# Performance work log

Measured on AMD Instinct MI355X. Metric: run time of the kernel, lower is better.

The kernel has to match this reference:

```python
import jax, jax.numpy as jnp
import numpy as np

HIDDEN = 3072
NUM_HEADS = 24
HEAD_DIM = HIDDEN // NUM_HEADS  # 128
MLP_HIDDEN = 4 * HIDDEN         # 12288
SEQ = 2048


def setup_inputs() -> dict:
    key = jax.random.key(0)
    ks = jax.random.split(key, 12)
    s = 0.02
    return {
        "x": jax.random.normal(ks[0], (1, SEQ, HIDDEN), jnp.float32),
        "vec": jax.random.normal(ks[1], (1, HIDDEN), jnp.float32),
        "pe": jax.random.normal(ks[2], (1, 1, SEQ, HEAD_DIM // 2, 2, 2), jnp.float32),
        "mod_w": jax.random.normal(ks[3], (HIDDEN, 3 * HIDDEN), jnp.float32) * s,
        "mod_b": jnp.zeros((3 * HIDDEN,), jnp.float32),
        "lin1_w": jax.random.normal(ks[4], (HIDDEN, 3 * HIDDEN + MLP_HIDDEN), jnp.float32) * s,
        "lin1_b": jnp.zeros((3 * HIDDEN + MLP_HIDDEN,), jnp.float32),
        "lin2_w": jax.random.normal(ks[5], (HIDDEN + MLP_HIDDEN, HIDDEN), jnp.float32) * s,
        "lin2_b": jnp.zeros((HIDDEN,), jnp.float32),
        "q_scale": jnp.ones((HEAD_DIM,), jnp.float32),
        "k_scale": jnp.ones((HEAD_DIM,), jnp.float32),
    }


def _forward(x, vec, pe, mod_w, mod_b, lin1_w, lin1_b, lin2_w, lin2_b, q_scale, k_scale):
    B, L, H = x.shape
    NH, HD = NUM_HEADS, HEAD_DIM

    # Modulation: lin(silu(vec)) -> shift, scale, gate  (flux Modulation, double=False)
    mod = jnp.dot(jax.nn.silu(vec), mod_w) + mod_b          # (B, 3H)
    shift, scale, gate = jnp.split(mod, 3, axis=-1)
    shift, scale, gate = shift[:, None, :], scale[:, None, :], gate[:, None, :]

    # LayerNorm (no affine, eps=1e-6) + scale/shift modulation
    mu = jnp.mean(x, axis=-1, keepdims=True)
    var = jnp.mean((x - mu) ** 2, axis=-1, keepdims=True)
    xn = (x - mu) * jax.lax.rsqrt(var + 1e-6)
    x_mod = (1.0 + scale) * xn + shift

    # Fused QKV + MLP projection
    h = jnp.dot(x_mod, lin1_w) + lin1_b                     # (B, L, 3H + MLP)
    qkv, mlp = h[..., : 3 * H], h[..., 3 * H :]
    qkv = qkv.reshape(B, L, 3, NH, HD).transpose(2, 0, 3, 1, 4)  # (3, B, NH, L, HD)
    q, k, v = qkv[0], qkv[1], qkv[2]

    # QKNorm: RMSNorm over head_dim with learned scale (eps=1e-6)
    def rms(t, s):
        return t * jax.lax.rsqrt(jnp.mean(t * t, axis=-1, keepdims=True) + 1e-6) * s

    q = rms(q, q_scale)
    k = rms(k, k_scale)

    # Rotary embedding: pe is (B, 1, L, HD/2, 2, 2) of rotation matrix rows
    def rope(t):
        tr = t.reshape(B, NH, L, HD // 2, 1, 2)
        out = pe[..., 0] * tr[..., 0] + pe[..., 1] * tr[..., 1]  # (B, NH, L, HD/2, 2)
        return out.reshape(B, NH, L, HD)

    q, k = rope(q), rope(k)

    # Scaled dot-product attention (default 1/sqrt(HD) scale)
    scores = jnp.einsum("bhqd,bhkd->bhqk", q, k) / jnp.sqrt(jnp.float32(HD))
    attn = jnp.einsum("bhqk,bhkd->bhqd", jax.nn.softmax(scores, axis=-1), v)
    attn = attn.transpose(0, 2, 1, 3).reshape(B, L, H)

    # GELU(tanh) MLP branch, concat, output projection, gated residual
    mlp_act = jax.nn.gelu(mlp, approximate=True)
    out = jnp.dot(jnp.concatenate([attn, mlp_act], axis=-1), lin2_w) + lin2_b
    return x + gate * out


def reference(x, vec, pe, mod_w, mod_b, lin1_w, lin1_b, lin2_w, lin2_b, q_scale, k_scale):
    return _forward(x, vec, pe, mod_w, mod_b, lin1_w, lin1_b, lin2_w, lin2_b, q_scale, k_scale)
```

## Files before the change

### kernel.cpp

```cpp
#include <hip/hip_runtime.h>
#include <hip/hip_bf16.h>
#include <stdint.h>

#define SEQ   2048
#define HID   3072
#define NHEADS 24
#define HDIM  128
#define MLPD  12288
#define NCOL1 21504
#define NCOL2 15360
#define MOD3  9216
#define QKVW  9216
#define KSPLIT 8

typedef __attribute__((ext_vector_type(4))) float f32x4;
typedef __attribute__((ext_vector_type(8))) short bf16x8;
typedef __attribute__((ext_vector_type(4))) unsigned short u16x4;
typedef __attribute__((ext_vector_type(2))) unsigned short u16x2;

__device__ __forceinline__ unsigned short f2bf(float f){
  unsigned u = __float_as_uint(f);
  u = (u + 0x7fffu + ((u >> 16) & 1u)) >> 16;
  return (unsigned short)u;
}
__device__ __forceinline__ float bf2f(unsigned short u){
  return __uint_as_float(((unsigned)u) << 16);
}

__device__ __forceinline__ void gload_lds16(const void* g, void* l){
  __builtin_amdgcn_global_load_lds(
      (const __attribute__((address_space(1))) unsigned int*)g,
      (__attribute__((address_space(3))) unsigned int*)l, 16, 0, 0);
}

__device__ __forceinline__ float gelu_tanh(float x){
  float u = 0.7978845608028654f * (x + 0.044715f * x * x * x);
  float t = 1.f - 2.f / (__expf(2.f * u) + 1.f);
  return 0.5f * x * (1.f + t);
}

__global__ void silu_kernel(const float* __restrict__ vec, float* __restrict__ sv){
  int i = blockIdx.x * 256 + threadIdx.x;
  if (i < HID){ float v = vec[i]; sv[i] = v / (1.f + __expf(-v)); }
}

__global__ void mod_gemv(const float* __restrict__ sv, const float* __restrict__ W,
                         const float* __restrict__ b, float* __restrict__ mod){
  int n  = blockIdx.x * 32 + (threadIdx.x & 31);
  int ks = threadIdx.x >> 5;
  float acc = 0.f;
  int k0 = ks * 384;
  #pragma unroll 4
  for (int k = k0; k < k0 + 384; ++k)
    acc += sv[k] * W[(size_t)k * MOD3 + n];
  __shared__ float red[8][32];
  red[ks][threadIdx.x & 31] = acc;
  __syncthreads();
  if (ks == 0){
    float a = 0.f;
    #pragma unroll
    for (int i = 0; i < 8; ++i) a += red[i][threadIdx.x & 31];
    mod[n] = a + b[n];
  }
}

__global__ __launch_bounds__(256)
void ln_mod_kernel(const float* __restrict__ x, const float* __restrict__ mod,
                   unsigned short* __restrict__ xmod){
  int l = blockIdx.x, t = threadIdx.x;
  const float* row = x + (size_t)l * HID;
  f32x4 v[3];
  float s = 0.f, s2 = 0.f;
  #pragma unroll
  for (int i = 0; i < 3; ++i){
    v[i] = *(const f32x4*)(row + (t + i * 256) * 4);
    #pragma unroll
    for (int j = 0; j < 4; ++j){ s += v[i][j]; s2 += v[i][j] * v[i][j]; }
  }
  #pragma unroll
  for (int m = 1; m < 64; m <<= 1){ s += __shfl_xor(s, m, 64); s2 += __shfl_xor(s2, m, 64); }
  __shared__ float red[8];
  int wv = t >> 6, ln = t & 63;
  if (ln == 0){ red[wv] = s; red[4 + wv] = s2; }
  __syncthreads();
  s  = red[0] + red[1] + red[2] + red[3];
  s2 = red[4] + red[5] + red[6] + red[7];
  float mu  = s * (1.f / HID);
  float var = s2 * (1.f / HID) - mu * mu;
  float rs  = rsqrtf(var + 1e-6f);
  #pragma unroll
  for (int i = 0; i < 3; ++i){
    int c = (t + i * 256) * 4;
    f32x4 sh = *(const f32x4*)(mod + c);
    f32x4 sc = *(const f32x4*)(mod + HID + c);
    u16x4 o;
    #pragma unroll
    for (int j = 0; j < 4; ++j){
      float xn = (v[i][j] - mu) * rs;
      o[j] = f2bf((1.f + sc[j]) * xn + sh[j]);
    }
    *(u16x4*)(xmod + (size_t)l * HID + c) = o;
  }
}

__global__ __launch_bounds__(256)
void transpose_f2b(const float* __restrict__ in, unsigned short* __restrict__ out,
                   int R, int C){
  __shared__ float tile[64][65];
  int rt = blockIdx.y * 64, ct = blockIdx.x * 64;
  int t = threadIdx.x;
  int r0 = t >> 4, c0 = (t & 15) * 4;
  #pragma unroll
  for (int ph = 0; ph < 4; ++ph){
    int r = r0 + ph * 16;
    f32x4 v = *(const f32x4*)(in + (size_t)(rt + r) * C + ct + c0);
    tile[r][c0 + 0] = v[0]; tile[r][c0 + 1] = v[1];
    tile[r][c0 + 2] = v[2]; tile[r][c0 + 3] = v[3];
  }
  __syncthreads();
  #pragma unroll
  for (int ph = 0; ph < 4; ++ph){
    int r = r0 + ph * 16;
    u16x4 o;
    #pragma unroll
    for (int i = 0; i < 4; ++i) o[i] = f2bf(tile[c0 + i][r]);
    *(u16x4*)(out + (size_t)(ct + r) * R + rt + c0) = o;
  }
}

__global__ __launch_bounds__(256)
void transpose_b2b_head(const unsigned short* __restrict__ in,
                        unsigned short* __restrict__ out, int R, int C){
  __shared__ unsigned short tile[64][68];
  int h = blockIdx.z;
  const unsigned short* inh = in + (size_t)h * R * C;
  unsigned short* outh = out + (size_t)h * R * C;
  int rt = blockIdx.y * 64, ct = blockIdx.x * 64;
  int t = threadIdx.x;
  int r0 = t >> 4, c0 = (t & 15) * 4;
  #pragma unroll
  for (int ph = 0; ph < 4; ++ph){
    int r = r0 + ph * 16;
    u16x4 v = *(const u16x4*)(inh + (size_t)(rt + r) * C + ct + c0);
    tile[r][c0 + 0] = v[0]; tile[r][c0 + 1] = v[1];
    tile[r][c0 + 2] = v[2]; tile[r][c0 + 3] = v[3];
  }
  __syncthreads();
  #pragma unroll
  for (int ph = 0; ph < 4; ++ph){
    int r = r0 + ph * 16;
    u16x4 o;
    #pragma unroll
    for (int i = 0; i < 4; ++i) o[i] = tile[c0 + i][r];
    *(u16x4*)(outh + (size_t)(ct + r) * R + rt + c0) = o;
  }
}

__global__ void qkv_prep(const unsigned short* __restrict__ hq, const float* __restrict__ pe,
                         const float* __restrict__ qscale, const float* __restrict__ kscale,
                         unsigned short* __restrict__ qb, unsigned short* __restrict__ kb,
                         unsigned short* __restrict__ vb){
  int l = blockIdx.x, hh = blockIdx.y, lane = threadIdx.x;
  const unsigned short* row = hq + (size_t)l * QKVW;
  int d = lane * 2;
  u16x2 qv = *(const u16x2*)(row + hh * HDIM + d);
  u16x2 kv = *(const u16x2*)(row + HID + hh * HDIM + d);
  u16x2 vv = *(const u16x2*)(row + 2 * HID + hh * HDIM + d);
  float qx = bf2f(qv[0]), qy = bf2f(qv[1]);
  float kx = bf2f(kv[0]), ky = bf2f(kv[1]);
  float sq = qx * qx + qy * qy;
  float sk = kx * kx + ky * ky;
  #pragma unroll
  for (int m = 1; m < 64; m <<= 1){ sq += __shfl_xor(sq, m, 64); sk += __shfl_xor(sk, m, 64); }
  float rq = rsqrtf(sq * (1.f / HDIM) + 1e-6f);
  float rk = rsqrtf(sk * (1.f / HDIM) + 1e-6f);
  float2 qs2 = *(const float2*)(qscale + d);
  float2 ks2 = *(const float2*)(kscale + d);
  float q0 = qx * rq * qs2.x, q1 = qy * rq * qs2.y;
  float k0 = kx * rk * ks2.x, k1 = ky * rk * ks2.y;
  f32x4 p4 = *(const f32x4*)(pe + (size_t)l * 256 + lane * 4);
  const float sscl = 0.08838834764831845f;
  float qo0 = (p4[0] * q0 + p4[1] * q1) * sscl;
  float qo1 = (p4[2] * q0 + p4[3] * q1) * sscl;
  float ko0 =  p4[0] * k0 + p4[1] * k1;
  float ko1 =  p4[2] * k0 + p4[3] * k1;
  size_t base = ((size_t)hh * SEQ + l) * HDIM + d;
  u16x2 o;
  o[0] = f2bf(qo0); o[1] = f2bf(qo1); *(u16x2*)(qb + base) = o;
  o[0] = f2bf(ko0); o[1] = f2bf(ko1); *(u16x2*)(kb + base) = o;
  o[0] = vv[0];     o[1] = vv[1];     *(u16x2*)(vb + base) = o;
}

template<int EPI>
__global__ __launch_bounds__(512)
void gemm256(const unsigned short* __restrict__ A, const unsigned short* __restrict__ BT,
             const float* __restrict__ bias, unsigned short* __restrict__ out0,
             unsigned short* __restrict__ out1,
             int M, int N, int ldA, int ldB, int kchunk){
  __shared__ unsigned short Ls[65536];
  int nxy = gridDim.x * gridDim.y;
  int nwg = nxy * gridDim.z;
  int fid = (blockIdx.z * gridDim.y + blockIdx.y) * gridDim.x + blockIdx.x;
  int nid = (fid & 7) * (nwg >> 3) + (fid >> 3);
  int ksz = nid / nxy, rem = nid % nxy;
  int bm  = rem % gridDim.y, bn = rem / gridDim.y;
  int k0 = ksz * kchunk;
  int nk = kchunk >> 6;
  int tid = threadIdx.x, wave = tid >> 6, lane = tid & 63, lg = lane >> 4, lr = lane & 15;
  int wr = wave >> 2, wc = wave & 3;

  int G0 = tid, G1 = tid + 512;
  int r0 = G0 >> 2, r1 = G1 >> 2;
  int c0 = ((G0 & 3) ^ ((r0 >> 1) & 3)) * 8;
  int c1 = ((G1 & 3) ^ ((r1 >> 1) & 3)) * 8;
  const unsigned short* A0 = A  + (size_t)(bm * 256 + r0) * ldA + k0 + c0;
  const unsigned short* A1 = A  + (size_t)(bm * 256 + r1) * ldA + k0 + c1;
  const unsigned short* B0 = BT + (size_t)(bn * 256 + r0) * ldB + k0 + c0;
  const unsigned short* B1 = BT + (size_t)(bn * 256 + r1) * ldB + k0 + c1;
  unsigned short* LA = Ls;
  unsigned short* LB = Ls + 32768;
  int d0 = (wave * 64) * 8, d1 = (512 + wave * 64) * 8;

  auto stageA = [&](int t, int kh){
    unsigned short* h = LA + (((t & 1) * 2 + kh) << 13);
    int kc = t * 64 + kh * 32;
    gload_lds16(A0 + kc, h + d0);
    gload_lds16(A1 + kc, h + d1);
  };
  auto stageB = [&](int t, int kh){
    unsigned short* h = LB + (((t & 1) * 2 + kh) << 13);
    int kc = t * 64 + kh * 32;
    gload_lds16(B0 + kc, h + d0);
    gload_lds16(B1 + kc, h + d1);
  };

  int offA[8], offB[4];
  #pragma unroll
  for (int m = 0; m < 8; ++m){
    int row = wr * 128 + m * 16 + lr;
    offA[m] = row * 32 + ((lg ^ ((row >> 1) & 3)) * 8);
  }
  #pragma unroll
  for (int n = 0; n < 4; ++n){
    int row = wc * 64 + n * 16 + lr;
    offB[n] = row * 32 + ((lg ^ ((row >> 1) & 3)) * 8);
  }

  const f32x4 fz = 0.0f;
  f32x4 acc[8][4];
  #pragma unroll
  for (int i = 0; i < 8; ++i)
    #pragma unroll
    for (int j = 0; j < 4; ++j) acc[i][j] = fz;

  stageA(0, 0); stageB(0, 0); stageA(0, 1); stageB(0, 1); stageA(1, 0); stageB(1, 0);
  asm volatile("s_waitcnt vmcnt(8)" ::: "memory");
  __builtin_amdgcn_s_barrier();
  __builtin_amdgcn_sched_barrier(0);

  for (int t = 0; t < nk; ++t){
    const unsigned short* Ah = LA + (((t & 1) * 2) << 13);
    const unsigned short* Bh = LB + (((t & 1) * 2) << 13);
    bf16x8 a_[4], b_[4];
    if (t + 1 < nk) stageA(t + 1, 1);
    #pragma unroll
    for (int m = 0; m < 4; ++m) a_[m] = *(const bf16x8*)&Ah[offA[m]];
    #pragma unroll
    for (int n = 0; n < 4; ++n) b_[n] = *(const bf16x8*)&Bh[offB[n]];
    __builtin_amdgcn_sched_barrier(0);
    __builtin_amdgcn_s_barrier();
    asm volatile("s_waitcnt lgkmcnt(0)" ::: "memory");
    __builtin_amdgcn_sched_barrier(0);
    __builtin_amdgcn_s_setprio(1);
    #pragma unroll
    for (int m = 0; m < 4; ++m)
      #pragma unroll
      for (int n = 0; n < 4; ++n)
        acc[m][n] = __builtin_amdgcn_mfma_f32_16x16x32_bf16(a_[m], b_[n], acc[m][n], 0, 0, 0);
    __builtin_amdgcn_s_setprio(0);
    __builtin_amdgcn_sched_barrier(0);
    __builtin_amdgcn_s_barrier();
    if (t + 1 < nk) stageB(t + 1, 1);
    #pragma unroll
    for (int m = 0; m < 4; ++m) a_[m] = *(const bf16x8*)&Ah[offA[m + 4]];
    __builtin_amdgcn_sched_barrier(0);
    if (t == nk - 1) asm volatile("s_waitcnt vmcnt(0)" ::: "memory");
    else             asm volatile("s_waitcnt vmcnt(8)" ::: "memory");
    __builtin_amdgcn_s_barrier();
    asm volatile("s_waitcnt lgkmcnt(0)" ::: "memory");
    __builtin_amdgcn_sched_barrier(0);
    __builtin_amdgcn_s_setprio(1);
    #pragma unroll
    for (int m = 0; m < 4; ++m)
      #pragma unroll
      for (int n = 0; n < 4; ++n)
        acc[m + 4][n] = __builtin_amdgcn_mfma_f32_16x16x32_bf16(a_[m], b_[n], acc[m + 4][n], 0, 0, 0);
    __builtin_amdgcn_s_setprio(0);
    __builtin_amdgcn_sched_barrier(0);
    __builtin_amdgcn_s_barrier();
    if (t + 2 < nk) stageA(t + 2, 0);
    #pragma unroll
    for (int m = 0; m < 4; ++m) a_[m] = *(const bf16x8*)&Ah[8192 + offA[m]];
    #pragma unroll
    for (int n = 0; n < 4; ++n) b_[n] = *(const bf16x8*)&Bh[8192 + offB[n]];
    __builtin_amdgcn_sched_barrier(0);
    __builtin_amdgcn_s_barrier();
    asm volatile("s_waitcnt lgkmcnt(0)" ::: "memory");
    __builtin_amdgcn_sched_barrier(0);
    __builtin_amdgcn_s_setprio(1);
    #pragma unroll
    for (int m = 0; m < 4; ++m)
      #pragma unroll
      for (int n = 0; n < 4; ++n)
        acc[m][n] = __builtin_amdgcn_mfma_f32_16x16x32_bf16(a_[m], b_[n], acc[m][n], 0, 0, 0);
    __builtin_amdgcn_s_setprio(0);
    __builtin_amdgcn_sched_barrier(0);
    __builtin_amdgcn_s_barrier();
    if (t + 2 < nk) stageB(t + 2, 0);
    #pragma unroll
    for (int m = 0; m < 4; ++m) a_[m] = *(const bf16x8*)&Ah[8192 + offA[m + 4]];
    __builtin_amdgcn_sched_barrier(0);
    if (t <= nk - 3)      asm volatile("s_waitcnt vmcnt(8)" ::: "memory");
    else if (t == nk - 2) asm volatile("s_waitcnt vmcnt(4)" ::: "memory");
    __builtin_amdgcn_s_barrier();
    asm volatile("s_waitcnt lgkmcnt(0)" ::: "memory");
    __builtin_amdgcn_sched_barrier(0);
    __builtin_amdgcn_s_setprio(1);
    #pragma unroll
    for (int m = 0; m < 4; ++m)
      #pragma unroll
      for (int n = 0; n < 4; ++n)
        acc[m + 4][n] = __builtin_amdgcn_mfma_f32_16x16x32_bf16(a_[m], b_[n], acc[m + 4][n], 0, 0, 0);
    __builtin_amdgcn_s_setprio(0);
    __builtin_amdgcn_sched_barrier(0);
    __builtin_amdgcn_s_barrier();
  }

  if constexpr (EPI == 0){
    if (bn < MOD3 / 256){
      #pragma unroll
      for (int m = 0; m < 8; ++m)
        #pragma unroll
        for (int n = 0; n < 4; ++n){
          int col = bn * 256 + wc * 64 + n * 16 + lr;
          float bv = bias[col];
          #pragma unroll
          for (int jj = 0; jj < 4; ++jj){
            int row = bm * 256 + wr * 128 + m * 16 + lg * 4 + jj;
            out0[(size_t)row * QKVW + col] = f2bf(acc[m][n][jj] + bv);
          }
        }
    } else {
      #pragma unroll
      for (int m = 0; m < 8; ++m)
        #pragma unroll
        for (int n = 0; n < 4; ++n){
          int col = bn * 256 + wc * 64 + n * 16 + lr;
          float bv = bias[col];
          #pragma unroll
          for (int jj = 0; jj < 4; ++jj){
            int row = bm * 256 + wr * 128 + m * 16 + lg * 4 + jj;
            out1[(size_t)row * NCOL2 + (col - 2 * HID)] = f2bf(gelu_tanh(acc[m][n][jj] + bv));
          }
        }
    }
  } else {
    unsigned short* P = out0 + (size_t)ksz * M * N;
    #pragma unroll
    for (int m = 0; m < 8; ++m)
      #pragma unroll
      for (int n = 0; n < 4; ++n){
        int col = bn * 256 + wc * 64 + n * 16 + lr;
        #pragma unroll
        for (int jj = 0; jj < 4; ++jj){
          int row = bm * 256 + wr * 128 + m * 16 + lg * 4 + jj;
          P[(size_t)row * N + col] = f2bf(acc[m][n][jj]);
        }
      }
  }
}

__global__ __launch_bounds__(256)
void reduce_lin2(const unsigned short* __restrict__ part, const float* __restrict__ x,
                 const float* __restrict__ gate, const float* __restrict__ bias,
                 float* __restrict__ out){
  int i4 = blockIdx.x * 256 + threadIdx.x;
  int c4 = i4 % (HID / 4);
  f32x4 s = 0.0f;
  #pragma unroll
  for (int ks = 0; ks < KSPLIT; ++ks){
    u16x4 p = *(const u16x4*)(part + (size_t)ks * SEQ * HID + (size_t)i4 * 4);
    #pragma unroll
    for (int j = 0; j < 4; ++j) s[j] += bf2f(p[j]);
  }
  f32x4 xv = *(const f32x4*)(x + (size_t)i4 * 4);
  f32x4 gv = *(const f32x4*)(gate + c4 * 4);
  f32x4 bv = *(const f32x4*)(bias + c4 * 4);
  f32x4 o;
  #pragma unroll
  for (int j = 0; j < 4; ++j) o[j] = xv[j] + gv[j] * (s[j] + bv[j]);
  *(f32x4*)(out + (size_t)i4 * 4) = o;
}

__global__ __launch_bounds__(256)
void attn_kernel(const unsigned short* __restrict__ qb, const unsigned short* __restrict__ kb,
                 const unsigned short* __restrict__ vt, unsigned short* __restrict__ a2){
  __shared__ unsigned short Ksm[64 * 128];
  __shared__ unsigned short Vsm[128 * 64];
  __shared__ unsigned short Psm[4][16 * 64];
  int fid = blockIdx.y * gridDim.x + blockIdx.x;
  int nid = (fid & 7) * 96 + (fid >> 3);
  int hh = nid / (SEQ / 64), qt = nid % (SEQ / 64);
  int tid = threadIdx.x, wave = tid >> 6, lane = tid & 63, lg = lane >> 4, lr = lane & 15;
  const unsigned short* Kh = kb + (size_t)hh * SEQ * HDIM;
  const unsigned short* Vh = vt + (size_t)hh * HDIM * SEQ;
  const unsigned short* Qh = qb + (size_t)hh * SEQ * HDIM;
  int q0 = qt * 64 + wave * 16;

  bf16x8 aq[4];
  #pragma unroll
  for (int kk = 0; kk < 4; ++kk)
    aq[kk] = *(const bf16x8*)(Qh + (size_t)(q0 + lr) * HDIM + kk * 32 + lg * 8);

  const f32x4 fzero = 0.0f;
  f32x4 acc_o[8];
  #pragma unroll
  for (int n = 0; n < 8; ++n) acc_o[n] = fzero;
  float mrun[4] = {-1e30f, -1e30f, -1e30f, -1e30f};
  float lrun[4] = {0.f, 0.f, 0.f, 0.f};

  for (int t = 0; t < SEQ / 64; ++t){
    __syncthreads();
    const unsigned short* Kt = Kh + (size_t)t * 64 * HDIM;
    const unsigned short* Vt = Vh + t * 64;
    #pragma unroll
    for (int r = 0; r < 4; ++r){
      int G  = r * 256 + tid;
      int Gs = G ^ ((G >> 4) & 7);
      gload_lds16(Kt + Gs * 8, (void*)&Ksm[(r * 256 + wave * 64) * 8]);
      int Gv = G ^ ((G >> 3) & 7);
      gload_lds16(Vt + (size_t)(Gv >> 3) * SEQ + (Gv & 7) * 8,
                  (void*)&Vsm[(r * 256 + wave * 64) * 8]);
    }
    __syncthreads();

    f32x4 sacc[4];
    #pragma unroll
    for (int j = 0; j < 4; ++j) sacc[j] = fzero;
    #pragma unroll
    for (int j = 0; j < 4; ++j){
      int kv = j * 16 + lr;
      #pragma unroll
      for (int kk = 0; kk < 4; ++kk){
        int bo = kv * 256 + (kk * 32 + lg * 8) * 2;
        bo ^= (kv & 7) << 4;
        bf16x8 bk = *(const bf16x8*)((const char*)Ksm + bo);
        sacc[j] = __builtin_amdgcn_mfma_f32_16x16x32_bf16(aq[kk], bk, sacc[j], 0, 0, 0);
      }
    }
    float scl[4], psum[4];
    #pragma unroll
    for (int jj = 0; jj < 4; ++jj){
      float m_ = fmaxf(fmaxf(sacc[0][jj], sacc[1][jj]), fmaxf(sacc[2][jj], sacc[3][jj]));
      #pragma unroll
      for (int mk = 1; mk < 16; mk <<= 1) m_ = fmaxf(m_, __shfl_xor(m_, mk, 64));
      float mn = fmaxf(mrun[jj], m_);
      scl[jj] = __expf(mrun[jj] - mn);
      mrun[jj] = mn;
      psum[jj] = 0.f;
    }
    #pragma unroll
    for (int j = 0; j < 4; ++j)
      #pragma unroll
      for (int jj = 0; jj < 4; ++jj){
        float p = __expf(sacc[j][jj] - mrun[jj]);
        sacc[j][jj] = p;
        psum[jj] += p;
      }
    #pragma unroll
    for (int jj = 0; jj < 4; ++jj){
      float ps = psum[jj];
      #pragma unroll
      for (int mk = 1; mk < 16; mk <<= 1) ps += __shfl_xor(ps, mk, 64);
      lrun[jj] = lrun[jj] * scl[jj] + ps;
    }
    #pragma unroll
    for (int n = 0; n < 8; ++n)
      #pragma unroll
      for (int jj = 0; jj < 4; ++jj) acc_o[n][jj] *= scl[jj];
    unsigned short* Pw = Psm[wave];
    #pragma unroll
    for (int j = 0; j < 4; ++j)
      #pragma unroll
      for (int jj = 0; jj < 4; ++jj){
        int prow = lg * 4 + jj, pcol = j * 16 + lr;
        int bo = prow * 128 + pcol * 2;
        bo ^= (prow & 7) << 4;
        *(unsigned short*)((char*)Pw + bo) = f2bf(sacc[j][jj]);
      }
    __syncthreads();
    #pragma unroll
    for (int k2 = 0; k2 < 2; ++k2){
      int bo = lr * 128 + (k2 * 32 + lg * 8) * 2;
      bo ^= (lr & 7) << 4;
      bf16x8 pf = *(const bf16x8*)((const char*)Pw + bo);
      #pragma unroll
      for (int n = 0; n < 8; ++n){
        int dd = n * 16 + lr;
        int vb_ = dd * 128 + (k2 * 32 + lg * 8) * 2;
        vb_ ^= (dd & 7) << 4;
        bf16x8 vf = *(const bf16x8*)((const char*)Vsm + vb_);
        acc_o[n] = __builtin_amdgcn_mfma_f32_16x16x32_bf16(pf, vf, acc_o[n], 0, 0, 0);
      }
    }
  }
  #pragma unroll
  for (int jj = 0; jj < 4; ++jj) lrun[jj] = 1.f / lrun[jj];
  #pragma unroll
  for (int n = 0; n < 8; ++n)
    #pragma unroll
    for (int jj = 0; jj < 4; ++jj){
      int row = q0 + lg * 4 + jj;
      int col = hh * HDIM + n * 16 + lr;
      a2[(size_t)row * NCOL2 + col] = f2bf(acc_o[n][jj] * lrun[jj]);
    }
}

extern "C" void kernel_launch(void* const* d_in, const int* in_sizes, int n_in,
                              void* d_out, int out_size, void* d_ws, size_t ws_size,
                              hipStream_t stream){
  const float* x       = (const float*)d_in[0];
  const float* vec     = (const float*)d_in[1];
  const float* pe      = (const float*)d_in[2];
  const float* mod_w   = (const float*)d_in[3];
  const float* mod_b   = (const float*)d_in[4];
  const float* lin1_w  = (const float*)d_in[5];
  const float* lin1_b  = (const float*)d_in[6];
  const float* lin2_w  = (const float*)d_in[7];
  const float* lin2_b  = (const float*)d_in[8];
  const float* q_scale = (const float*)d_in[9];
  const float* k_scale = (const float*)d_in[10];
  float* out = (float*)d_out;

  char* ws = (char*)d_ws;
  size_t off = 0;
  auto alloc = [&](size_t bytes){ void* p = ws + off; off += (bytes + 255) & ~(size_t)255; return p; };
  float* sv            = (float*)alloc((size_t)HID * 4);
  float* mod           = (float*)alloc((size_t)MOD3 * 4);
  unsigned short* xmod = (unsigned short*)alloc((size_t)SEQ * HID * 2);
  unsigned short* wt2  = (unsigned short*)alloc((size_t)HID * NCOL2 * 2);
  unsigned short* a2   = (unsigned short*)alloc((size_t)SEQ * NCOL2 * 2);
  unsigned short* qb   = (unsigned short*)alloc((size_t)NHEADS * SEQ * HDIM * 2);
  unsigned short* kb   = (unsigned short*)alloc((size_t)NHEADS * SEQ * HDIM * 2);
  unsigned short* vb   = (unsigned short*)alloc((size_t)NHEADS * SEQ * HDIM * 2);
  unsigned short* vt   = (unsigned short*)alloc((size_t)NHEADS * SEQ * HDIM * 2);
  unsigned short* wt1  = (unsigned short*)alloc((size_t)NCOL1 * HID * 2);
  unsigned short* hq   = (unsigned short*)alloc((size_t)SEQ * QKVW * 2);
  unsigned short* part = qb;

  silu_kernel<<<12, 256, 0, stream>>>(vec, sv);
  mod_gemv<<<MOD3 / 32, 256, 0, stream>>>(sv, mod_w, mod_b, mod);
  transpose_f2b<<<dim3(NCOL1 / 64, HID / 64), 256, 0, stream>>>(lin1_w, wt1, HID, NCOL1);
  transpose_f2b<<<dim3(HID / 64, NCOL2 / 64), 256, 0, stream>>>(lin2_w, wt2, NCOL2, HID);
  ln_mod_kernel<<<SEQ, 256, 0, stream>>>(x, mod, xmod);
  gemm256<0><<<dim3(NCOL1 / 256, SEQ / 256, 1), 512, 0, stream>>>(
      xmod, wt1, lin1_b, hq, a2, SEQ, NCOL1, HID, HID, HID);
  qkv_prep<<<dim3(SEQ, NHEADS), 64, 0, stream>>>(hq, pe, q_scale, k_scale, qb, kb, vb);
  transpose_b2b_head<<<dim3(HDIM / 64, SEQ / 64, NHEADS), 256, 0, stream>>>(vb, vt, SEQ, HDIM);
  attn_kernel<<<dim3(SEQ / 64, NHEADS), 256, 0, stream>>>(qb, kb, vt, a2);
  gemm256<2><<<dim3(HID / 256, SEQ / 256, KSPLIT), 512, 0, stream>>>(
      a2, wt2, nullptr, part, nullptr, SEQ, HID, NCOL2, NCOL2, NCOL2 / KSPLIT);
  reduce_lin2<<<SEQ * HID / 4 / 256, 256, 0, stream>>>(part, x, mod + 2 * HID, lin2_b, out);
}
```

Before: 847.1 us.

## Use 256x192 tiles for lin2 GEMM with split-K reduced to four

The GEMM kernel now takes the number of N-fragments per wave as a template parameter, so the lin2 projection uses 256x192 tiles (16 column tiles) with split-K of 4 in place of 256x256 tiles with split-K of 8. The B tile staging masks off the extra threads and adjusts the vmcnt waits to match. The aim is to halve the partial-sum traffic written by the GEMM and read by the reduction while keeping a similar workgroup count (512 rather than 768). In exchange each workgroup does fewer MFMAs per A-tile load, which lowers arithmetic intensity.

```diff
diff --git a/kernel.cpp b/kernel.cpp
--- a/kernel.cpp
+++ b/kernel.cpp
@@ -11,12 +11,14 @@
 #define NCOL2 15360
 #define MOD3  9216
 #define QKVW  9216
-#define KSPLIT 8
+#define KS2   4
 
 typedef __attribute__((ext_vector_type(4))) float f32x4;
 typedef __attribute__((ext_vector_type(8))) short bf16x8;
 typedef __attribute__((ext_vector_type(4))) unsigned short u16x4;
 typedef __attribute__((ext_vector_type(2))) unsigned short u16x2;
+
+#define VMC(n) asm volatile("s_waitcnt vmcnt(" #n ")" ::: "memory")
 
 __device__ __forceinline__ unsigned short f2bf(float f){
   unsigned u = __float_as_uint(f);
@@ -191,13 +193,17 @@
   o[0] = vv[0];     o[1] = vv[1];     *(u16x2*)(vb + base) = o;
 }
 
-template<int EPI>
+template<int NFRAG, int EPI>
 __global__ __launch_bounds__(512)
 void gemm256(const unsigned short* __restrict__ A, const unsigned short* __restrict__ BT,
              const float* __restrict__ bias, unsigned short* __restrict__ out0,
              unsigned short* __restrict__ out1,
              int M, int N, int ldA, int ldB, int kchunk){
-  __shared__ unsigned short Ls[65536];
+  constexpr int BN  = NFRAG * 64;
+  constexpr int BGT = BN * 2;
+  constexpr int HB  = BN * 32;
+  __shared__ unsigned short As[4 * 8192];
+  __shared__ unsigned short Bs[4 * HB];
   int nxy = gridDim.x * gridDim.y;
   int nwg = nxy * gridDim.z;
   int fid = (blockIdx.z * gridDim.y + blockIdx.y) * gridDim.x + blockIdx.x;
@@ -209,64 +215,67 @@
   int tid = threadIdx.x, wave = tid >> 6, lane = tid & 63, lg = lane >> 4, lr = lane & 15;
   int wr = wave >> 2, wc = wave & 3;
 
-  int G0 = tid, G1 = tid + 512;
-  int r0 = G0 >> 2, r1 = G1 >> 2;
-  int c0 = ((G0 & 3) ^ ((r0 >> 1) & 3)) * 8;
-  int c1 = ((G1 & 3) ^ ((r1 >> 1) & 3)) * 8;
-  const unsigned short* A0 = A  + (size_t)(bm * 256 + r0) * ldA + k0 + c0;
-  const unsigned short* A1 = A  + (size_t)(bm * 256 + r1) * ldA + k0 + c1;
-  const unsigned short* B0 = BT + (size_t)(bn * 256 + r0) * ldB + k0 + c0;
-  const unsigned short* B1 = BT + (size_t)(bn * 256 + r1) * ldB + k0 + c1;
-  unsigned short* LA = Ls;
-  unsigned short* LB = Ls + 32768;
+  int rA0 = tid >> 2, rA1 = (tid + 512) >> 2;
+  int cA0 = ((tid & 3) ^ ((rA0 >> 1) & 3)) * 8;
+  int cA1 = ((tid & 3) ^ ((rA1 >> 1) & 3)) * 8;
+  const unsigned short* A0 = A + (size_t)(bm * 256 + rA0) * ldA + k0 + cA0;
+  const unsigned short* A1 = A + (size_t)(bm * 256 + rA1) * ldA + k0 + cA1;
+  int rB0 = tid >> 2, rB1 = (tid + BGT) >> 2;
+  int cB1 = ((tid & 3) ^ ((rB1 >> 1) & 3)) * 8;
+  const unsigned short* B0 = BT + (size_t)(bn * BN + rB0) * ldB + k0 + cA0;
+  const unsigned short* B1 = BT + (size_t)(bn * BN + rB1) * ldB + k0 + cB1;
   int d0 = (wave * 64) * 8, d1 = (512 + wave * 64) * 8;
+  int dB1 = (BGT + wave * 64) * 8;
+  bool bact = (BGT == 512) || (tid < BGT);
 
   auto stageA = [&](int t, int kh){
-    unsigned short* h = LA + (((t & 1) * 2 + kh) << 13);
+    unsigned short* h = As + (((t & 1) * 2 + kh) << 13);
     int kc = t * 64 + kh * 32;
     gload_lds16(A0 + kc, h + d0);
     gload_lds16(A1 + kc, h + d1);
   };
   auto stageB = [&](int t, int kh){
-    unsigned short* h = LB + (((t & 1) * 2 + kh) << 13);
-    int kc = t * 64 + kh * 32;
-    gload_lds16(B0 + kc, h + d0);
-    gload_lds16(B1 + kc, h + d1);
+    if (bact){
+      unsigned short* h = Bs + ((t & 1) * 2 + kh) * HB;
+      int kc = t * 64 + kh * 32;
+      gload_lds16(B0 + kc, h + d0);
+      gload_lds16(B1 + kc, h + dB1);
+    }
   };
 
-  int offA[8], offB[4];
+  int offA[8], offB[NFRAG];
   #pragma unroll
   for (int m = 0; m < 8; ++m){
     int row = wr * 128 + m * 16 + lr;
     offA[m] = row * 32 + ((lg ^ ((row >> 1) & 3)) * 8);
   }
   #pragma unroll
-  for (int n = 0; n < 4; ++n){
-    int row = wc * 64 + n * 16 + lr;
+  for (int n = 0; n < NFRAG; ++n){
+    int row = wc * (NFRAG * 16) + n * 16 + lr;
     offB[n] = row * 32 + ((lg ^ ((row >> 1) & 3)) * 8);
   }
 
   const f32x4 fz = 0.0f;
-  f32x4 acc[8][4];
+  f32x4 acc[8][NFRAG];
   #pragma unroll
   for (int i = 0; i < 8; ++i)
     #pragma unroll
-    for (int j = 0; j < 4; ++j) acc[i][j] = fz;
+    for (int j = 0; j < NFRAG; ++j) acc[i][j] = fz;
 
   stageA(0, 0); stageB(0, 0); stageA(0, 1); stageB(0, 1); stageA(1, 0); stageB(1, 0);
-  asm volatile("s_waitcnt vmcnt(8)" ::: "memory");
+  if (bact) VMC(8); else VMC(4);
   __builtin_amdgcn_s_barrier();
   __builtin_amdgcn_sched_barrier(0);
 
   for (int t = 0; t < nk; ++t){
-    const unsigned short* Ah = LA + (((t & 1) * 2) << 13);
-    const unsigned short* Bh = LB + (((t & 1) * 2) << 13);
-    bf16x8 a_[4], b_[4];
+    const unsigned short* Ah = As + (((t & 1) * 2) << 13);
+    const unsigned short* Bh = Bs + ((t & 1) * 2) * HB;
+    bf16x8 a_[4], b_[NFRAG];
     if (t + 1 < nk) stageA(t + 1, 1);
     #pragma unroll
     for (int m = 0; m < 4; ++m) a_[m] = *(const bf16x8*)&Ah[offA[m]];
     #pragma unroll
-    for (int n = 0; n < 4; ++n) b_[n] = *(const bf16x8*)&Bh[offB[n]];
+    for (int n = 0; n < NFRAG; ++n) b_[n] = *(const bf16x8*)&Bh[offB[n]];
     __builtin_amdgcn_sched_barrier(0);
     __builtin_amdgcn_s_barrier();
     asm volatile("s_waitcnt lgkmcnt(0)" ::: "memory");
@@ -275,7 +284,7 @@
     #pragma unroll
     for (int m = 0; m < 4; ++m)
       #pragma unroll
-      for (int n = 0; n < 4; ++n)
+      for (int n = 0; n < NFRAG; ++n)
         acc[m][n] = __builtin_amdgcn_mfma_f32_16x16x32_bf16(a_[m], b_[n], acc[m][n], 0, 0, 0);
     __builtin_amdgcn_s_setprio(0);
     __builtin_amdgcn_sched_barrier(0);
@@ -284,8 +293,8 @@
     #pragma unroll
     for (int m = 0; m < 4; ++m) a_[m] = *(const bf16x8*)&Ah[offA[m + 4]];
     __builtin_amdgcn_sched_barrier(0);
-    if (t == nk - 1) asm volatile("s_waitcnt vmcnt(0)" ::: "memory");
-    else             asm volatile("s_waitcnt vmcnt(8)" ::: "memory");
+    if (t == nk - 1){ VMC(0); }
+    else            { if (bact) VMC(8); else VMC(4); }
     __builtin_amdgcn_s_barrier();
     asm volatile("s_waitcnt lgkmcnt(0)" ::: "memory");
     __builtin_amdgcn_sched_barrier(0);
@@ -293,7 +302,7 @@
     #pragma unroll
     for (int m = 0; m < 4; ++m)
       #pragma unroll
-      for (int n = 0; n < 4; ++n)
+      for (int n = 0; n < NFRAG; ++n)
         acc[m + 4][n] = __builtin_amdgcn_mfma_f32_16x16x32_bf16(a_[m], b_[n], acc[m + 4][n], 0, 0, 0);
     __builtin_amdgcn_s_setprio(0);
     __builtin_amdgcn_sched_barrier(0);
@@ -302,7 +311,7 @@
     #pragma unroll
     for (int m = 0; m < 4; ++m) a_[m] = *(const bf16x8*)&Ah[8192 + offA[m]];
     #pragma unroll
-    for (int n = 0; n < 4; ++n) b_[n] = *(const bf16x8*)&Bh[8192 + offB[n]];
+    for (int n = 0; n < NFRAG; ++n) b_[n] = *(const bf16x8*)&Bh[HB + offB[n]];
     __builtin_amdgcn_sched_barrier(0);
     __builtin_amdgcn_s_barrier();
     asm volatile("s_waitcnt lgkmcnt(0)" ::: "memory");
@@ -311,7 +320,7 @@
     #pragma unroll
     for (int m = 0; m < 4; ++m)
       #pragma unroll
-      for (int n = 0; n < 4; ++n)
+      for (int n = 0; n < NFRAG; ++n)
         acc[m][n] = __builtin_amdgcn_mfma_f32_16x16x32_bf16(a_[m], b_[n], acc[m][n], 0, 0, 0);
     __builtin_amdgcn_s_setprio(0);
     __builtin_amdgcn_sched_barrier(0);
@@ -320,8 +329,8 @@
     #pragma unroll
     for (int m = 0; m < 4; ++m) a_[m] = *(const bf16x8*)&Ah[8192 + offA[m + 4]];
     __builtin_amdgcn_sched_barrier(0);
-    if (t <= nk - 3)      asm volatile("s_waitcnt vmcnt(8)" ::: "memory");
-    else if (t == nk - 2) asm volatile("s_waitcnt vmcnt(4)" ::: "memory");
+    if (t <= nk - 3)      { if (bact) VMC(8); else VMC(4); }
+    else if (t == nk - 2) { if (bact) VMC(4); else VMC(2); }
     __builtin_amdgcn_s_barrier();
     asm volatile("s_waitcnt lgkmcnt(0)" ::: "memory");
     __builtin_amdgcn_sched_barrier(0);
@@ -329,7 +338,7 @@
     #pragma unroll
     for (int m = 0; m < 4; ++m)
       #pragma unroll
-      for (int n = 0; n < 4; ++n)
+      for (int n = 0; n < NFRAG; ++n)
         acc[m + 4][n] = __builtin_amdgcn_mfma_f32_16x16x32_bf16(a_[m], b_[n], acc[m + 4][n], 0, 0, 0);
     __builtin_amdgcn_s_setprio(0);
     __builtin_amdgcn_sched_barrier(0);
@@ -337,12 +346,12 @@
   }
 
   if constexpr (EPI == 0){
-    if (bn < MOD3 / 256){
+    if (bn < MOD3 / BN){
       #pragma unroll
       for (int m = 0; m < 8; ++m)
         #pragma unroll
-        for (int n = 0; n < 4; ++n){
-          int col = bn * 256 + wc * 64 + n * 16 + lr;
+        for (int n = 0; n < NFRAG; ++n){
+          int col = bn * BN + wc * (NFRAG * 16) + n * 16 + lr;
           float bv = bias[col];
           #pragma unroll
           for (int jj = 0; jj < 4; ++jj){
@@ -354,8 +363,8 @@
       #pragma unroll
       for (int m = 0; m < 8; ++m)
         #pragma unroll
-        for (int n = 0; n < 4; ++n){
-          int col = bn * 256 + wc * 64 + n * 16 + lr;
+        for (int n = 0; n < NFRAG; ++n){
+          int col = bn * BN + wc * (NFRAG * 16) + n * 16 + lr;
           float bv = bias[col];
           #pragma unroll
           for (int jj = 0; jj < 4; ++jj){
@@ -369,8 +378,8 @@
     #pragma unroll
     for (int m = 0; m < 8; ++m)
       #pragma unroll
-      for (int n = 0; n < 4; ++n){
-        int col = bn * 256 + wc * 64 + n * 16 + lr;
+      for (int n = 0; n < NFRAG; ++n){
+        int col = bn * BN + wc * (NFRAG * 16) + n * 16 + lr;
         #pragma unroll
         for (int jj = 0; jj < 4; ++jj){
           int row = bm * 256 + wr * 128 + m * 16 + lg * 4 + jj;
@@ -388,7 +397,7 @@
   int c4 = i4 % (HID / 4);
   f32x4 s = 0.0f;
   #pragma unroll
-  for (int ks = 0; ks < KSPLIT; ++ks){
+  for (int ks = 0; ks < KS2; ++ks){
     u16x4 p = *(const u16x4*)(part + (size_t)ks * SEQ * HID + (size_t)i4 * 4);
     #pragma unroll
     for (int j = 0; j < 4; ++j) s[j] += bf2f(p[j]);
@@ -563,12 +572,12 @@
   transpose_f2b<<<dim3(NCOL1 / 64, HID / 64), 256, 0, stream>>>(lin1_w, wt1, HID, NCOL1);
   transpose_f2b<<<dim3(HID / 64, NCOL2 / 64), 256, 0, stream>>>(lin2_w, wt2, NCOL2, HID);
   ln_mod_kernel<<<SEQ, 256, 0, stream>>>(x, mod, xmod);
-  gemm256<0><<<dim3(NCOL1 / 256, SEQ / 256, 1), 512, 0, stream>>>(
+  gemm256<4, 0><<<dim3(NCOL1 / 256, SEQ / 256, 1), 512, 0, stream>>>(
       xmod, wt1, lin1_b, hq, a2, SEQ, NCOL1, HID, HID, HID);
   qkv_prep<<<dim3(SEQ, NHEADS), 64, 0, stream>>>(hq, pe, q_scale, k_scale, qb, kb, vb);
   transpose_b2b_head<<<dim3(HDIM / 64, SEQ / 64, NHEADS), 256, 0, stream>>>(vb, vt, SEQ, HDIM);
   attn_kernel<<<dim3(SEQ / 64, NHEADS), 256, 0, stream>>>(qb, kb, vt, a2);
-  gemm256<2><<<dim3(HID / 256, SEQ / 256, KSPLIT), 512, 0, stream>>>(
-      a2, wt2, nullptr, part, nullptr, SEQ, HID, NCOL2, NCOL2, NCOL2 / KSPLIT);
+  gemm256<3, 2><<<dim3(NCOL2 / NCOL2 * 16, SEQ / 256, KS2), 512, 0, stream>>>(
+      a2, wt2, nullptr, part, nullptr, SEQ, HID, NCOL2, NCOL2, NCOL2 / KS2);
   reduce_lin2<<<SEQ * HID / 4 / 256, 256, 0, stream>>>(part, x, mod + 2 * HID, lin2_b, out);
 }
```

After: 1.037 ms. 1.22x slower.
